# Performance work log

Hardware: AMD Instinct MI355X
Metric: run time of the kernel (lower is better)

Reference implementation:

```python
import jax, jax.numpy as jnp
import numpy as np

N = 100000
E = 800000
D = 128


def setup_inputs() -> dict:
    key = jax.random.key(0)
    ks = jax.random.split(key, 12)
    s = 1.0 / np.sqrt(D)
    return {
        "x": jax.random.normal(ks[0], (N, D), dtype=jnp.float32),
        "edge_index": jax.random.randint(ks[1], (2, E), 0, N, dtype=jnp.int64),
        "W_proj": jax.random.normal(ks[2], (D, D), dtype=jnp.float32) * s,
        "W1_l": jax.random.normal(ks[3], (D, D), dtype=jnp.float32) * s,
        "b1": jnp.zeros((D,), dtype=jnp.float32),
        "W1_r": jax.random.normal(ks[4], (D, D), dtype=jnp.float32) * s,
        "W2_l": jax.random.normal(ks[5], (D, D), dtype=jnp.float32) * s,
        "b2": jnp.zeros((D,), dtype=jnp.float32),
        "W2_r": jax.random.normal(ks[6], (D, D), dtype=jnp.float32) * s,
        "W3_l": jax.random.normal(ks[7], (D, D), dtype=jnp.float32) * s,
        "b3": jnp.zeros((D,), dtype=jnp.float32),
        "W3_r": jax.random.normal(ks[8], (D, D), dtype=jnp.float32) * s,
    }


def _sage_conv(x, src, dst, deg_inv, W_l, b, W_r):
    # scatter-mean aggregation of neighbor (source) features onto destinations
    agg = jax.ops.segment_sum(x[src], dst, num_segments=N)  # [N, D]
    mean = agg * deg_inv[:, None]
    # out = lin_l(mean) + lin_r(x); PyG Linear: y = x @ W.T (+ b on lin_l only)
    return mean @ W_l.T + b + x @ W_r.T


def reference(x, edge_index, W_proj, W1_l, b1, W1_r, W2_l, b2, W2_r, W3_l, b3, W3_r):
    src = edge_index[0]
    dst = edge_index[1]
    deg = jax.ops.segment_sum(jnp.ones((E,), dtype=x.dtype), dst, num_segments=N)
    deg_inv = jnp.where(deg > 0, 1.0 / jnp.maximum(deg, 1.0), 0.0)

    identity = x
    h = x @ W_proj.T
    h = _sage_conv(h, src, dst, deg_inv, W1_l, b1, W1_r)
    h = jax.nn.relu(h)
    h = h + identity  # dropout is identity at inference

    identity = h
    h = _sage_conv(h, src, dst, deg_inv, W2_l, b2, W2_r)
    h = jax.nn.relu(h)
    h = h + identity

    h = _sage_conv(h, src, dst, deg_inv, W3_l, b3, W3_r)
    # F.normalize(dim=1): x / max(||x||_2, eps)
    norm = jnp.sqrt(jnp.sum(h * h, axis=1, keepdims=True))
    return h / jnp.maximum(norm, 1e-12)
```

## Files before the change

### kernel.cpp

```cpp
#include <hip/hip_runtime.h>

typedef unsigned int uint;
typedef unsigned short ushort;
typedef float f32x4 __attribute__((ext_vector_type(4)));
typedef short short8 __attribute__((ext_vector_type(8)));

#define DIMS 128
#define SCAN_B 1024

__device__ __forceinline__ ushort f2bf(float f) {
    uint u = __builtin_bit_cast(uint, f);
    u += 0x7fffu + ((u >> 16) & 1u);
    return (ushort)(u >> 16);
}
__device__ __forceinline__ float bf2f(ushort h) {
    uint u = (uint)h << 16;
    return __builtin_bit_cast(float, u);
}


__global__ __launch_bounds__(256) void hist_kernel(const int* __restrict__ dst,
                                                   int* __restrict__ deg, int E) {
    int i = blockIdx.x * 256 + threadIdx.x;
    if (i < E) atomicAdd(&deg[dst[i]], 1);
}

__global__ __launch_bounds__(256) void scan_reduce(const int* __restrict__ deg,
                                                   int* __restrict__ bsum, int n) {
    __shared__ int s[256];
    const int t = threadIdx.x;
    const int base = blockIdx.x * SCAN_B;
    int v = 0;
#pragma unroll
    for (int j = 0; j < 4; ++j) {
        int i = base + t * 4 + j;
        if (i < n) v += deg[i];
    }
    s[t] = v;
    __syncthreads();
    for (int off = 128; off > 0; off >>= 1) {
        if (t < off) s[t] += s[t + off];
        __syncthreads();
    }
    if (t == 0) bsum[blockIdx.x] = s[0];
}

__global__ __launch_bounds__(256) void scan_bsum(int* __restrict__ bsum, int nb) {
    __shared__ int s[256];
    const int t = threadIdx.x;
    int v = (t < nb) ? bsum[t] : 0;
    s[t] = v;
    __syncthreads();
    for (int off = 1; off < 256; off <<= 1) {
        int u = (t >= off) ? s[t - off] : 0;
        __syncthreads();
        s[t] += u;
        __syncthreads();
    }
    if (t < nb) bsum[t] = s[t] - v;
}

__global__ __launch_bounds__(256) void scan_final(const int* __restrict__ deg,
                                                  const int* __restrict__ bsum,
                                                  int* __restrict__ row_start,
                                                  float* __restrict__ deg_inv, int n) {
    __shared__ int s[256];
    const int t = threadIdx.x;
    const int base = blockIdx.x * SCAN_B;
    int loc[4];
    int v = 0;
#pragma unroll
    for (int j = 0; j < 4; ++j) {
        int i = base + t * 4 + j;
        loc[j] = (i < n) ? deg[i] : 0;
        v += loc[j];
    }
    s[t] = v;
    __syncthreads();
    for (int off = 1; off < 256; off <<= 1) {
        int u = (t >= off) ? s[t - off] : 0;
        __syncthreads();
        s[t] += u;
        __syncthreads();
    }
    int excl = bsum[blockIdx.x] + s[t] - v;
#pragma unroll
    for (int j = 0; j < 4; ++j) {
        int i = base + t * 4 + j;
        if (i < n) {
            row_start[i] = excl;
            deg_inv[i] = loc[j] > 0 ? 1.0f / (float)loc[j] : 0.0f;
        }
        excl += loc[j];
        if (i == n - 1) row_start[n] = excl;
    }
}

__global__ __launch_bounds__(256) void fill_kernel(const int* __restrict__ src,
                                                   const int* __restrict__ dst,
                                                   const int* __restrict__ row_start,
                                                   int* __restrict__ cursor,
                                                   int* __restrict__ col_idx, int E) {
    int i = blockIdx.x * 256 + threadIdx.x;
    if (i < E) {
        int d = dst[i];
        int pos = atomicAdd(&cursor[d], 1);
        col_idx[row_start[d] + pos] = src[i];
    }
}


__global__ __launch_bounds__(256) void wconv_kernel(const float* __restrict__ W0,
                                                    const float* __restrict__ W1,
                                                    const float* __restrict__ W2,
                                                    const float* __restrict__ W3,
                                                    const float* __restrict__ W4,
                                                    const float* __restrict__ W5,
                                                    const float* __restrict__ W6,
                                                    ushort* __restrict__ wbuf) {
    const float* W;
    switch (blockIdx.y) {
        case 0: W = W0; break;
        case 1: W = W1; break;
        case 2: W = W2; break;
        case 3: W = W3; break;
        case 4: W = W4; break;
        case 5: W = W5; break;
        default: W = W6; break;
    }
    int idx = blockIdx.x * 256 + threadIdx.x;
    int g = idx >> 6;
    int l = idx & 63;
    int nt = g >> 2, c = g & 3;
    int m15 = l & 15, kg = l >> 4;
    int r = nt * 16 + m15;
    int k0 = c * 32 + kg * 8;
    f32x4 f0 = *(const f32x4*)(W + r * DIMS + k0);
    f32x4 f1 = *(const f32x4*)(W + r * DIMS + k0 + 4);
    short8 v;
    v[0] = (short)f2bf(f0[0]); v[1] = (short)f2bf(f0[1]);
    v[2] = (short)f2bf(f0[2]); v[3] = (short)f2bf(f0[3]);
    v[4] = (short)f2bf(f1[0]); v[5] = (short)f2bf(f1[1]);
    v[6] = (short)f2bf(f1[2]); v[7] = (short)f2bf(f1[3]);
    *(short8*)(wbuf + (size_t)blockIdx.y * 16384 + g * 512 + l * 8) = v;
}


template <int ABF16, int DUAL>
__global__ __launch_bounds__(512) void gemm_mfma(const void* __restrict__ Xv,
                                                 const ushort* __restrict__ wbuf,
                                                 ushort* __restrict__ Ya,
                                                 ushort* __restrict__ Yb, int n) {
    __shared__ ushort wlds[(DUAL ? 2 : 1) * 16384];

    const int t = threadIdx.x;
    const int l = t & 63;
    const int w = t >> 6;
    const int kg = l >> 4;
    const int m15 = l & 15;

    const int NITER = DUAL ? 8 : 4;
#pragma unroll
    for (int it = 0; it < NITER; ++it) {
        int g = it * 8 + w;
        short8 v = *(const short8*)(wbuf + (size_t)g * 512 + l * 8);
        *(short8*)((char*)wlds + g * 1024 + l * 16) = v;
    }

    const int row0 = blockIdx.x * 128;
    const int arow = row0 + w * 16 + m15;
    short8 af[4];
    if (arow < n) {
#pragma unroll
        for (int c = 0; c < 4; ++c) {
            if (ABF16) {
                const ushort* X = (const ushort*)Xv;
                af[c] = *(const short8*)(X + (size_t)arow * DIMS + c * 32 + kg * 8);
            } else {
                const float* X = (const float*)Xv;
                f32x4 f0 = *(const f32x4*)(X + (size_t)arow * DIMS + c * 32 + kg * 8);
                f32x4 f1 = *(const f32x4*)(X + (size_t)arow * DIMS + c * 32 + kg * 8 + 4);
                short8 v;
                v[0] = (short)f2bf(f0[0]); v[1] = (short)f2bf(f0[1]);
                v[2] = (short)f2bf(f0[2]); v[3] = (short)f2bf(f0[3]);
                v[4] = (short)f2bf(f1[0]); v[5] = (short)f2bf(f1[1]);
                v[6] = (short)f2bf(f1[2]); v[7] = (short)f2bf(f1[3]);
                af[c] = v;
            }
        }
    } else {
#pragma unroll
        for (int c = 0; c < 4; ++c) af[c] = (short8){};
    }

    __syncthreads();

    f32x4 accA[8] = {};
    f32x4 accB[8] = {};
#pragma unroll
    for (int c = 0; c < 4; ++c) {
#pragma unroll
        for (int nt = 0; nt < 8; ++nt) {
            short8 bA = *(const short8*)((const char*)wlds + (nt * 4 + c) * 1024 + l * 16);
            accA[nt] = __builtin_amdgcn_mfma_f32_16x16x32_bf16(af[c], bA, accA[nt], 0, 0, 0);
            if (DUAL) {
                short8 bB = *(const short8*)((const char*)wlds + (32 + nt * 4 + c) * 1024 + l * 16);
                accB[nt] = __builtin_amdgcn_mfma_f32_16x16x32_bf16(af[c], bB, accB[nt], 0, 0, 0);
            }
        }
    }

    __syncthreads();
    const int r0 = w * 16 + (l >> 4) * 4;
    ushort* outA = (ushort*)wlds;
    ushort* outB = outA + 16384;
#pragma unroll
    for (int nt = 0; nt < 8; ++nt) {
#pragma unroll
        for (int j = 0; j < 4; ++j) {
            outA[(r0 + j) * DIMS + nt * 16 + m15] = f2bf(accA[nt][j]);
            if (DUAL) outB[(r0 + j) * DIMS + nt * 16 + m15] = f2bf(accB[nt][j]);
        }
    }
    __syncthreads();
#pragma unroll
    for (int i = 0; i < 4; ++i) {
        int idx = i * 512 + t;
        int row = idx >> 4;
        int col = (idx & 15) * 8;
        if (row0 + row < n) {
            *(short8*)(Ya + (size_t)(row0 + row) * DIMS + col) = *(const short8*)(outA + idx * 8);
            if (DUAL)
                *(short8*)(Yb + (size_t)(row0 + row) * DIMS + col) = *(const short8*)(outB + idx * 8);
        }
    }
}


__global__ __launch_bounds__(256) void aggregate_kernel(
    const ushort* __restrict__ yl, const ushort* __restrict__ yr,
    const float* __restrict__ bias, const void* __restrict__ identity, int idf32,
    const int* __restrict__ row_start, const int* __restrict__ col_idx,
    const float* __restrict__ deg_inv, float* __restrict__ out_f32,
    ushort* __restrict__ out_bf16, int n, int mode) {
    const int wv = threadIdx.x >> 6;
    const int lane = threadIdx.x & 63;
    const int node = blockIdx.x * 4 + wv;
    if (node >= n) return;
    const int grp = lane >> 4;
    const int sl = lane & 15;

    const int s = row_start[node];
    const int cnt = row_start[node + 1] - s;

    float f[8] = {};
    for (int p0 = 0; p0 < cnt; p0 += 64) {
        int m = cnt - p0;
        if (m > 64) m = 64;
        int cv = (p0 + lane < cnt) ? col_idx[s + p0 + lane] : 0;
        for (int j = 0; j < m; j += 4) {
            int c = __shfl(cv, j + grp);
            if (j + grp < m) {
                short8 v = *(const short8*)(yl + (size_t)c * DIMS + sl * 8);
#pragma unroll
                for (int q = 0; q < 8; ++q) f[q] += bf2f((ushort)v[q]);
            }
        }
    }
#pragma unroll
    for (int q = 0; q < 8; ++q) {
        f[q] += __shfl_xor(f[q], 16);
        f[q] += __shfl_xor(f[q], 32);
    }

    const float di = deg_inv[node];
    f32x4 b0 = *(const f32x4*)(bias + sl * 8);
    f32x4 b1 = *(const f32x4*)(bias + sl * 8 + 4);
    short8 rv = *(const short8*)(yr + (size_t)node * DIMS + sl * 8);
    float h[8];
#pragma unroll
    for (int q = 0; q < 8; ++q)
        h[q] = fmaf(f[q], di, (q < 4 ? b0[q] : b1[q - 4])) + bf2f((ushort)rv[q]);

    if (mode == 0) {
        if (idf32) {
            const float* idp = (const float*)identity + (size_t)node * DIMS + sl * 8;
            f32x4 i0 = *(const f32x4*)idp;
            f32x4 i1 = *(const f32x4*)(idp + 4);
#pragma unroll
            for (int q = 0; q < 8; ++q)
                h[q] = fmaxf(h[q], 0.f) + (q < 4 ? i0[q] : i1[q - 4]);
        } else {
            short8 iv = *(const short8*)((const ushort*)identity + (size_t)node * DIMS + sl * 8);
#pragma unroll
            for (int q = 0; q < 8; ++q) h[q] = fmaxf(h[q], 0.f) + bf2f((ushort)iv[q]);
        }
    } else {
        float ss = 0.f;
#pragma unroll
        for (int q = 0; q < 8; ++q) ss += h[q] * h[q];
        ss += __shfl_xor(ss, 1);
        ss += __shfl_xor(ss, 2);
        ss += __shfl_xor(ss, 4);
        ss += __shfl_xor(ss, 8);
        float inv = 1.0f / fmaxf(sqrtf(ss), 1e-12f);
#pragma unroll
        for (int q = 0; q < 8; ++q) h[q] *= inv;
    }

    if (grp == 0) {
        if (out_bf16) {
            short8 o;
#pragma unroll
            for (int q = 0; q < 8; ++q) o[q] = (short)f2bf(h[q]);
            *(short8*)(out_bf16 + (size_t)node * DIMS + sl * 8) = o;
        }
        if (out_f32) {
            f32x4 o0, o1;
#pragma unroll
            for (int q = 0; q < 4; ++q) { o0[q] = h[q]; o1[q] = h[q + 4]; }
            *(f32x4*)(out_f32 + (size_t)node * DIMS + sl * 8) = o0;
            *(f32x4*)(out_f32 + (size_t)node * DIMS + sl * 8 + 4) = o1;
        }
    }
}


extern "C" void kernel_launch(void* const* d_in, const int* in_sizes, int n_in,
                              void* d_out, int out_size, void* d_ws, size_t ws_size,
                              hipStream_t stream) {
    const float* x     = (const float*)d_in[0];
    const int*   eidx  = (const int*)d_in[1];
    const float* Wproj = (const float*)d_in[2];
    const float* W1_l  = (const float*)d_in[3];
    const float* b1    = (const float*)d_in[4];
    const float* W1_r  = (const float*)d_in[5];
    const float* W2_l  = (const float*)d_in[6];
    const float* b2    = (const float*)d_in[7];
    const float* W2_r  = (const float*)d_in[8];
    const float* W3_l  = (const float*)d_in[9];
    const float* b3    = (const float*)d_in[10];
    const float* W3_r  = (const float*)d_in[11];
    float* out = (float*)d_out;

    const int N = in_sizes[0] / DIMS;
    const int E = in_sizes[1] / 2;
    const int* src = eidx;
    const int* dst = eidx + E;

    size_t off = 0;
    auto alloc = [&](size_t bytes) {
        void* p = (char*)d_ws + off;
        off += (bytes + 511) & ~(size_t)511;
        return p;
    };
    int*    deg_cnt   = (int*)alloc((size_t)N * 4);
    int*    cursor    = (int*)alloc((size_t)N * 4);
    int*    row_start = (int*)alloc((size_t)(N + 1) * 4);
    float*  deg_inv   = (float*)alloc((size_t)N * 4);
    int*    col_idx   = (int*)alloc((size_t)E * 4);
    int*    bsum      = (int*)alloc((size_t)1024 * 4);
    ushort* wbuf      = (ushort*)alloc((size_t)7 * 16384 * 2);
    ushort* h0b       = (ushort*)alloc((size_t)N * DIMS * 2);
    ushort* h1b       = (ushort*)alloc((size_t)N * DIMS * 2);
    ushort* ylb       = (ushort*)alloc((size_t)N * DIMS * 2);
    ushort* yrb       = (ushort*)alloc((size_t)N * DIMS * 2);
    ushort* h2b       = h0b;
    (void)ws_size;

    hipMemsetAsync(deg_cnt, 0, (size_t)N * 4, stream);
    hipMemsetAsync(cursor, 0, (size_t)N * 4, stream);

    const int egrid = (E + 255) / 256;
    const int sgrid = (N + SCAN_B - 1) / SCAN_B;
    const int ggrid = (N + 127) / 128;
    const int agrid = (N + 3) / 4;

    hist_kernel<<<egrid, 256, 0, stream>>>(dst, deg_cnt, E);
    scan_reduce<<<sgrid, 256, 0, stream>>>(deg_cnt, bsum, N);
    scan_bsum<<<1, 256, 0, stream>>>(bsum, sgrid);
    scan_final<<<sgrid, 256, 0, stream>>>(deg_cnt, bsum, row_start, deg_inv, N);
    fill_kernel<<<egrid, 256, 0, stream>>>(src, dst, row_start, cursor, col_idx, E);
    wconv_kernel<<<dim3(8, 7), 256, 0, stream>>>(Wproj, W1_l, W1_r, W2_l, W2_r, W3_l, W3_r,
                                                 wbuf);

    gemm_mfma<0, 0><<<ggrid, 512, 0, stream>>>(x, wbuf, h0b, nullptr, N);

    gemm_mfma<1, 1><<<ggrid, 512, 0, stream>>>(h0b, wbuf + 1 * 16384, ylb, yrb, N);
    aggregate_kernel<<<agrid, 256, 0, stream>>>(ylb, yrb, b1, x, 1, row_start, col_idx,
                                                deg_inv, nullptr, h1b, N, 0);

    gemm_mfma<1, 1><<<ggrid, 512, 0, stream>>>(h1b, wbuf + 3 * 16384, ylb, yrb, N);
    aggregate_kernel<<<agrid, 256, 0, stream>>>(ylb, yrb, b2, h1b, 0, row_start, col_idx,
                                                deg_inv, nullptr, h2b, N, 0);

    gemm_mfma<1, 1><<<ggrid, 512, 0, stream>>>(h2b, wbuf + 5 * 16384, ylb, yrb, N);
    aggregate_kernel<<<agrid, 256, 0, stream>>>(ylb, yrb, b3, nullptr, 0, row_start, col_idx,
                                                deg_inv, out, nullptr, N, 1);
}
```

Before: 417.7 us.

## Aggregate before transform and fuse lin_l/lin_r into one K=256 GEMM epilogue

Reorders each SAGE layer so mean aggregation runs on the input features first. A single GEMM then concatenates [mean, h] along K (256) against stacked [W_l; W_r], and applies bias, ReLU, residual or L2-normalize in its epilogue. This removes the separate yr buffer and its write/read and the per-layer dual output. The aggregate kernel now only writes the bf16 mean. The first GEMM also emits a bf16 copy of x for the residual, which changes the identity from fp32 to bf16 and adds a little rounding. A swizzled fp32 LDS tile is used for the epilogue.

```diff
diff --git a/kernel.cpp b/kernel.cpp
--- a/kernel.cpp
+++ b/kernel.cpp
@@ -110,48 +110,64 @@
 }
 
 
-__global__ __launch_bounds__(256) void wconv_kernel(const float* __restrict__ W0,
-                                                    const float* __restrict__ W1,
-                                                    const float* __restrict__ W2,
-                                                    const float* __restrict__ W3,
-                                                    const float* __restrict__ W4,
-                                                    const float* __restrict__ W5,
-                                                    const float* __restrict__ W6,
+__global__ __launch_bounds__(256) void wconv_kernel(const float* __restrict__ Wp,
+                                                    const float* __restrict__ W1l,
+                                                    const float* __restrict__ W1r,
+                                                    const float* __restrict__ W2l,
+                                                    const float* __restrict__ W2r,
+                                                    const float* __restrict__ W3l,
+                                                    const float* __restrict__ W3r,
                                                     ushort* __restrict__ wbuf) {
-    const float* W;
-    switch (blockIdx.y) {
-        case 0: W = W0; break;
-        case 1: W = W1; break;
-        case 2: W = W2; break;
-        case 3: W = W3; break;
-        case 4: W = W4; break;
-        case 5: W = W5; break;
-        default: W = W6; break;
-    }
+    const int y = blockIdx.y;
     int idx = blockIdx.x * 256 + threadIdx.x;
-    int g = idx >> 6;
     int l = idx & 63;
-    int nt = g >> 2, c = g & 3;
     int m15 = l & 15, kg = l >> 4;
-    int r = nt * 16 + m15;
-    int k0 = c * 32 + kg * 8;
-    f32x4 f0 = *(const f32x4*)(W + r * DIMS + k0);
-    f32x4 f1 = *(const f32x4*)(W + r * DIMS + k0 + 4);
-    short8 v;
-    v[0] = (short)f2bf(f0[0]); v[1] = (short)f2bf(f0[1]);
-    v[2] = (short)f2bf(f0[2]); v[3] = (short)f2bf(f0[3]);
-    v[4] = (short)f2bf(f1[0]); v[5] = (short)f2bf(f1[1]);
-    v[6] = (short)f2bf(f1[2]); v[7] = (short)f2bf(f1[3]);
-    *(short8*)(wbuf + (size_t)blockIdx.y * 16384 + g * 512 + l * 8) = v;
-}
-
-
-template <int ABF16, int DUAL>
-__global__ __launch_bounds__(512) void gemm_mfma(const void* __restrict__ Xv,
-                                                 const ushort* __restrict__ wbuf,
-                                                 ushort* __restrict__ Ya,
-                                                 ushort* __restrict__ Yb, int n) {
-    __shared__ ushort wlds[(DUAL ? 2 : 1) * 16384];
+    if (y == 0) {
+        if (idx >= 2048) return;
+        int g = idx >> 6;
+        int nt = g >> 2, c = g & 3;
+        int r = nt * 16 + m15;
+        int k0 = c * 32 + kg * 8;
+        f32x4 f0 = *(const f32x4*)(Wp + r * DIMS + k0);
+        f32x4 f1 = *(const f32x4*)(Wp + r * DIMS + k0 + 4);
+        short8 v;
+        v[0] = (short)f2bf(f0[0]); v[1] = (short)f2bf(f0[1]);
+        v[2] = (short)f2bf(f0[2]); v[3] = (short)f2bf(f0[3]);
+        v[4] = (short)f2bf(f1[0]); v[5] = (short)f2bf(f1[1]);
+        v[6] = (short)f2bf(f1[2]); v[7] = (short)f2bf(f1[3]);
+        *(short8*)(wbuf + (size_t)g * 512 + l * 8) = v;
+    } else {
+        const float* Wl = (y == 1) ? W1l : (y == 2) ? W2l : W3l;
+        const float* Wr = (y == 1) ? W1r : (y == 2) ? W2r : W3r;
+        int g = idx >> 6;
+        int nt = g >> 3, c = g & 7;
+        int r = nt * 16 + m15;
+        int k = c * 32 + kg * 8;
+        const float* W = (k < 128) ? Wl : Wr;
+        int kk = k & 127;
+        f32x4 f0 = *(const f32x4*)(W + r * DIMS + kk);
+        f32x4 f1 = *(const f32x4*)(W + r * DIMS + kk + 4);
+        short8 v;
+        v[0] = (short)f2bf(f0[0]); v[1] = (short)f2bf(f0[1]);
+        v[2] = (short)f2bf(f0[2]); v[3] = (short)f2bf(f0[3]);
+        v[4] = (short)f2bf(f1[0]); v[5] = (short)f2bf(f1[1]);
+        v[6] = (short)f2bf(f1[2]); v[7] = (short)f2bf(f1[3]);
+        *(short8*)(wbuf + 16384 + (size_t)(y - 1) * 32768 + (size_t)g * 512 + l * 8) = v;
+    }
+}
+
+
+template <int MODE>
+__global__ __launch_bounds__(512) void gemm_fused(const void* __restrict__ Xa,
+                                                  const ushort* __restrict__ Xh,
+                                                  const ushort* __restrict__ wbuf,
+                                                  const float* __restrict__ bias,
+                                                  const ushort* __restrict__ idb,
+                                                  ushort* __restrict__ Ya,
+                                                  ushort* __restrict__ Yb,
+                                                  float* __restrict__ outf, int n) {
+    constexpr int NC = (MODE == 0) ? 4 : 8;
+    __shared__ ushort wlds[32768];
 
     const int t = threadIdx.x;
     const int l = t & 63;
@@ -159,9 +175,8 @@
     const int kg = l >> 4;
     const int m15 = l & 15;
 
-    const int NITER = DUAL ? 8 : 4;
-#pragma unroll
-    for (int it = 0; it < NITER; ++it) {
+#pragma unroll
+    for (int it = 0; it < NC; ++it) {
         int g = it * 8 + w;
         short8 v = *(const short8*)(wbuf + (size_t)g * 512 + l * 8);
         *(short8*)((char*)wlds + g * 1024 + l * 16) = v;
@@ -169,15 +184,12 @@
 
     const int row0 = blockIdx.x * 128;
     const int arow = row0 + w * 16 + m15;
-    short8 af[4];
+    short8 af[NC];
     if (arow < n) {
-#pragma unroll
-        for (int c = 0; c < 4; ++c) {
-            if (ABF16) {
-                const ushort* X = (const ushort*)Xv;
-                af[c] = *(const short8*)(X + (size_t)arow * DIMS + c * 32 + kg * 8);
-            } else {
-                const float* X = (const float*)Xv;
+        if (MODE == 0) {
+            const float* X = (const float*)Xa;
+#pragma unroll
+            for (int c = 0; c < 4; ++c) {
                 f32x4 f0 = *(const f32x4*)(X + (size_t)arow * DIMS + c * 32 + kg * 8);
                 f32x4 f1 = *(const f32x4*)(X + (size_t)arow * DIMS + c * 32 + kg * 8 + 4);
                 short8 v;
@@ -187,62 +199,115 @@
                 v[6] = (short)f2bf(f1[2]); v[7] = (short)f2bf(f1[3]);
                 af[c] = v;
             }
+        } else {
+            const ushort* Xm = (const ushort*)Xa;
+#pragma unroll
+            for (int c = 0; c < 4; ++c)
+                af[c] = *(const short8*)(Xm + (size_t)arow * DIMS + c * 32 + kg * 8);
+#pragma unroll
+            for (int c = 0; c < 4; ++c)
+                af[4 + c] = *(const short8*)(Xh + (size_t)arow * DIMS + c * 32 + kg * 8);
         }
     } else {
 #pragma unroll
-        for (int c = 0; c < 4; ++c) af[c] = (short8){};
+        for (int c = 0; c < NC; ++c) af[c] = (short8){};
     }
 
     __syncthreads();
 
-    f32x4 accA[8] = {};
-    f32x4 accB[8] = {};
-#pragma unroll
-    for (int c = 0; c < 4; ++c) {
+    f32x4 acc[8] = {};
+#pragma unroll
+    for (int c = 0; c < NC; ++c)
 #pragma unroll
         for (int nt = 0; nt < 8; ++nt) {
-            short8 bA = *(const short8*)((const char*)wlds + (nt * 4 + c) * 1024 + l * 16);
-            accA[nt] = __builtin_amdgcn_mfma_f32_16x16x32_bf16(af[c], bA, accA[nt], 0, 0, 0);
-            if (DUAL) {
-                short8 bB = *(const short8*)((const char*)wlds + (32 + nt * 4 + c) * 1024 + l * 16);
-                accB[nt] = __builtin_amdgcn_mfma_f32_16x16x32_bf16(af[c], bB, accB[nt], 0, 0, 0);
-            }
-        }
-    }
+            short8 b = *(const short8*)((const char*)wlds + (nt * NC + c) * 1024 + l * 16);
+            acc[nt] = __builtin_amdgcn_mfma_f32_16x16x32_bf16(af[c], b, acc[nt], 0, 0, 0);
+        }
 
     __syncthreads();
     const int r0 = w * 16 + (l >> 4) * 4;
-    ushort* outA = (ushort*)wlds;
-    ushort* outB = outA + 16384;
-#pragma unroll
-    for (int nt = 0; nt < 8; ++nt) {
-#pragma unroll
-        for (int j = 0; j < 4; ++j) {
-            outA[(r0 + j) * DIMS + nt * 16 + m15] = f2bf(accA[nt][j]);
-            if (DUAL) outB[(r0 + j) * DIMS + nt * 16 + m15] = f2bf(accB[nt][j]);
-        }
-    }
-    __syncthreads();
-#pragma unroll
-    for (int i = 0; i < 4; ++i) {
-        int idx = i * 512 + t;
-        int row = idx >> 4;
-        int col = (idx & 15) * 8;
-        if (row0 + row < n) {
-            *(short8*)(Ya + (size_t)(row0 + row) * DIMS + col) = *(const short8*)(outA + idx * 8);
-            if (DUAL)
+
+    if (MODE == 0) {
+        ushort* outA = wlds;
+        ushort* outB = wlds + 16384;
+#pragma unroll
+        for (int nt = 0; nt < 8; ++nt)
+#pragma unroll
+            for (int j = 0; j < 4; ++j)
+                outA[(r0 + j) * DIMS + nt * 16 + m15] = f2bf(acc[nt][j]);
+        const int rl = w * 16 + m15;
+#pragma unroll
+        for (int c = 0; c < 4; ++c)
+            *(short8*)(outB + rl * DIMS + c * 32 + kg * 8) = af[c];
+        __syncthreads();
+#pragma unroll
+        for (int i = 0; i < 4; ++i) {
+            int idx = i * 512 + t;
+            int row = idx >> 4, col = (idx & 15) * 8;
+            if (row0 + row < n) {
+                *(short8*)(Ya + (size_t)(row0 + row) * DIMS + col) = *(const short8*)(outA + idx * 8);
                 *(short8*)(Yb + (size_t)(row0 + row) * DIMS + col) = *(const short8*)(outB + idx * 8);
-        }
-    }
-}
-
-
-__global__ __launch_bounds__(256) void aggregate_kernel(
-    const ushort* __restrict__ yl, const ushort* __restrict__ yr,
-    const float* __restrict__ bias, const void* __restrict__ identity, int idf32,
-    const int* __restrict__ row_start, const int* __restrict__ col_idx,
-    const float* __restrict__ deg_inv, float* __restrict__ out_f32,
-    ushort* __restrict__ out_bf16, int n, int mode) {
+            }
+        }
+    } else {
+        float* outF = (float*)wlds;
+#pragma unroll
+        for (int nt = 0; nt < 8; ++nt)
+#pragma unroll
+            for (int j = 0; j < 4; ++j) {
+                int row = r0 + j;
+                int col = nt * 16 + m15;
+                int sc = (((col >> 2) ^ (row & 7)) << 2) | (col & 3);
+                outF[row * DIMS + sc] = acc[nt][j];
+            }
+        __syncthreads();
+#pragma unroll
+        for (int i = 0; i < 4; ++i) {
+            int idx = i * 512 + t;
+            int row = idx >> 4, col = (idx & 15) * 8;
+            if (row0 + row < n) {
+                int x7 = row & 7;
+                int cb = col >> 2;
+                f32x4 o0 = *(const f32x4*)(outF + row * DIMS + ((cb ^ x7) << 2));
+                f32x4 o1 = *(const f32x4*)(outF + row * DIMS + (((cb + 1) ^ x7) << 2));
+                f32x4 b0 = *(const f32x4*)(bias + col);
+                f32x4 b1 = *(const f32x4*)(bias + col + 4);
+                float h[8];
+#pragma unroll
+                for (int q = 0; q < 4; ++q) { h[q] = o0[q] + b0[q]; h[4 + q] = o1[q] + b1[q]; }
+                if (MODE == 1) {
+                    short8 iv = *(const short8*)(idb + (size_t)(row0 + row) * DIMS + col);
+                    short8 o;
+#pragma unroll
+                    for (int q = 0; q < 8; ++q)
+                        o[q] = (short)f2bf(fmaxf(h[q], 0.f) + bf2f((ushort)iv[q]));
+                    *(short8*)(Ya + (size_t)(row0 + row) * DIMS + col) = o;
+                } else {
+                    float ss = 0.f;
+#pragma unroll
+                    for (int q = 0; q < 8; ++q) ss += h[q] * h[q];
+                    ss += __shfl_xor(ss, 1);
+                    ss += __shfl_xor(ss, 2);
+                    ss += __shfl_xor(ss, 4);
+                    ss += __shfl_xor(ss, 8);
+                    float inv = 1.0f / fmaxf(sqrtf(ss), 1e-12f);
+                    f32x4 o0s, o1s;
+#pragma unroll
+                    for (int q = 0; q < 4; ++q) { o0s[q] = h[q] * inv; o1s[q] = h[4 + q] * inv; }
+                    *(f32x4*)(outf + (size_t)(row0 + row) * DIMS + col) = o0s;
+                    *(f32x4*)(outf + (size_t)(row0 + row) * DIMS + col + 4) = o1s;
+                }
+            }
+        }
+    }
+}
+
+
+__global__ __launch_bounds__(256) void agg_mean(const ushort* __restrict__ hsrc,
+                                                const int* __restrict__ row_start,
+                                                const int* __restrict__ col_idx,
+                                                const float* __restrict__ deg_inv,
+                                                ushort* __restrict__ mean, int n) {
     const int wv = threadIdx.x >> 6;
     const int lane = threadIdx.x & 63;
     const int node = blockIdx.x * 4 + wv;
@@ -261,7 +326,7 @@
         for (int j = 0; j < m; j += 4) {
             int c = __shfl(cv, j + grp);
             if (j + grp < m) {
-                short8 v = *(const short8*)(yl + (size_t)c * DIMS + sl * 8);
+                short8 v = *(const short8*)(hsrc + (size_t)c * DIMS + sl * 8);
 #pragma unroll
                 for (int q = 0; q < 8; ++q) f[q] += bf2f((ushort)v[q]);
             }
@@ -272,56 +337,12 @@
         f[q] += __shfl_xor(f[q], 16);
         f[q] += __shfl_xor(f[q], 32);
     }
-
-    const float di = deg_inv[node];
-    f32x4 b0 = *(const f32x4*)(bias + sl * 8);
-    f32x4 b1 = *(const f32x4*)(bias + sl * 8 + 4);
-    short8 rv = *(const short8*)(yr + (size_t)node * DIMS + sl * 8);
-    float h[8];
-#pragma unroll
-    for (int q = 0; q < 8; ++q)
-        h[q] = fmaf(f[q], di, (q < 4 ? b0[q] : b1[q - 4])) + bf2f((ushort)rv[q]);
-
-    if (mode == 0) {
-        if (idf32) {
-            const float* idp = (const float*)identity + (size_t)node * DIMS + sl * 8;
-            f32x4 i0 = *(const f32x4*)idp;
-            f32x4 i1 = *(const f32x4*)(idp + 4);
-#pragma unroll
-            for (int q = 0; q < 8; ++q)
-                h[q] = fmaxf(h[q], 0.f) + (q < 4 ? i0[q] : i1[q - 4]);
-        } else {
-            short8 iv = *(const short8*)((const ushort*)identity + (size_t)node * DIMS + sl * 8);
-#pragma unroll
-            for (int q = 0; q < 8; ++q) h[q] = fmaxf(h[q], 0.f) + bf2f((ushort)iv[q]);
-        }
-    } else {
-        float ss = 0.f;
-#pragma unroll
-        for (int q = 0; q < 8; ++q) ss += h[q] * h[q];
-        ss += __shfl_xor(ss, 1);
-        ss += __shfl_xor(ss, 2);
-        ss += __shfl_xor(ss, 4);
-        ss += __shfl_xor(ss, 8);
-        float inv = 1.0f / fmaxf(sqrtf(ss), 1e-12f);
-#pragma unroll
-        for (int q = 0; q < 8; ++q) h[q] *= inv;
-    }
-
     if (grp == 0) {
-        if (out_bf16) {
-            short8 o;
-#pragma unroll
-            for (int q = 0; q < 8; ++q) o[q] = (short)f2bf(h[q]);
-            *(short8*)(out_bf16 + (size_t)node * DIMS + sl * 8) = o;
-        }
-        if (out_f32) {
-            f32x4 o0, o1;
-#pragma unroll
-            for (int q = 0; q < 4; ++q) { o0[q] = h[q]; o1[q] = h[q + 4]; }
-            *(f32x4*)(out_f32 + (size_t)node * DIMS + sl * 8) = o0;
-            *(f32x4*)(out_f32 + (size_t)node * DIMS + sl * 8 + 4) = o1;
-        }
+        const float di = deg_inv[node];
+        short8 o;
+#pragma unroll
+        for (int q = 0; q < 8; ++q) o[q] = (short)f2bf(f[q] * di);
+        *(short8*)(mean + (size_t)node * DIMS + sl * 8) = o;
     }
 }
 
@@ -360,12 +381,12 @@
     float*  deg_inv   = (float*)alloc((size_t)N * 4);
     int*    col_idx   = (int*)alloc((size_t)E * 4);
     int*    bsum      = (int*)alloc((size_t)1024 * 4);
-    ushort* wbuf      = (ushort*)alloc((size_t)7 * 16384 * 2);
-    ushort* h0b       = (ushort*)alloc((size_t)N * DIMS * 2);
-    ushort* h1b       = (ushort*)alloc((size_t)N * DIMS * 2);
-    ushort* ylb       = (ushort*)alloc((size_t)N * DIMS * 2);
-    ushort* yrb       = (ushort*)alloc((size_t)N * DIMS * 2);
-    ushort* h2b       = h0b;
+    ushort* wbuf      = (ushort*)alloc((size_t)(16384 + 3 * 32768) * 2);
+    ushort* xb        = (ushort*)alloc((size_t)N * DIMS * 2);
+    ushort* h0        = (ushort*)alloc((size_t)N * DIMS * 2);
+    ushort* h1        = (ushort*)alloc((size_t)N * DIMS * 2);
+    ushort* mbuf      = (ushort*)alloc((size_t)N * DIMS * 2);
+    ushort* h2        = h0;
     (void)ws_size;
 
     hipMemsetAsync(deg_cnt, 0, (size_t)N * 4, stream);
@@ -375,26 +396,29 @@
     const int sgrid = (N + SCAN_B - 1) / SCAN_B;
     const int ggrid = (N + 127) / 128;
     const int agrid = (N + 3) / 4;
+
+    const ushort* w1 = wbuf + 16384;
+    const ushort* w2 = wbuf + 16384 + 32768;
+    const ushort* w3 = wbuf + 16384 + 2 * 32768;
 
     hist_kernel<<<egrid, 256, 0, stream>>>(dst, deg_cnt, E);
     scan_reduce<<<sgrid, 256, 0, stream>>>(deg_cnt, bsum, N);
     scan_bsum<<<1, 256, 0, stream>>>(bsum, sgrid);
     scan_final<<<sgrid, 256, 0, stream>>>(deg_cnt, bsum, row_start, deg_inv, N);
     fill_kernel<<<egrid, 256, 0, stream>>>(src, dst, row_start, cursor, col_idx, E);
-    wconv_kernel<<<dim3(8, 7), 256, 0, stream>>>(Wproj, W1_l, W1_r, W2_l, W2_r, W3_l, W3_r,
-                                                 wbuf);
-
-    gemm_mfma<0, 0><<<ggrid, 512, 0, stream>>>(x, wbuf, h0b, nullptr, N);
-
-    gemm_mfma<1, 1><<<ggrid, 512, 0, stream>>>(h0b, wbuf + 1 * 16384, ylb, yrb, N);
-    aggregate_kernel<<<agrid, 256, 0, stream>>>(ylb, yrb, b1, x, 1, row_start, col_idx,
-                                                deg_inv, nullptr, h1b, N, 0);
-
-    gemm_mfma<1, 1><<<ggrid, 512, 0, stream>>>(h1b, wbuf + 3 * 16384, ylb, yrb, N);
-    aggregate_kernel<<<agrid, 256, 0, stream>>>(ylb, yrb, b2, h1b, 0, row_start, col_idx,
-                                                deg_inv, nullptr, h2b, N, 0);
-
-    gemm_mfma<1, 1><<<ggrid, 512, 0, stream>>>(h2b, wbuf + 5 * 16384, ylb, yrb, N);
-    aggregate_kernel<<<agrid, 256, 0, stream>>>(ylb, yrb, b3, nullptr, 0, row_start, col_idx,
-                                                deg_inv, out, nullptr, N, 1);
-}
+    wconv_kernel<<<dim3(16, 4), 256, 0, stream>>>(Wproj, W1_l, W1_r, W2_l, W2_r, W3_l, W3_r,
+                                                  wbuf);
+
+    gemm_fused<0><<<ggrid, 512, 0, stream>>>(x, nullptr, wbuf, nullptr, nullptr,
+                                             h0, xb, nullptr, N);
+
+    agg_mean<<<agrid, 256, 0, stream>>>(h0, row_start, col_idx, deg_inv, mbuf, N);
+    gemm_fused<1><<<ggrid, 512, 0, stream>>>(mbuf, h0, w1, b1, xb, h1, nullptr, nullptr, N);
+
+    agg_mean<<<agrid, 256, 0, stream>>>(h1, row_start, col_idx, deg_inv, mbuf, N);
+    gemm_fused<1><<<ggrid, 512, 0, stream>>>(mbuf, h1, w2, b2, h1, h2, nullptr, nullptr, N);
+
+    agg_mean<<<agrid, 256, 0, stream>>>(h2, row_start, col_idx, deg_inv, mbuf, N);
+    gemm_fused<2><<<ggrid, 512, 0, stream>>>(mbuf, h2, w3, b3, nullptr, nullptr, nullptr,
+                                             out, N);
+}
```

New measurement: 407.3 us. -2.5%, faster.
